# Kernel optimization log

Hardware: AMD Instinct MI355X
Metric: run time of the kernel (lower is better)

The kernel has to match this reference:

```python
import jax, jax.numpy as jnp
import numpy as np

N = 50000      # nodes
E = 1_600_000  # edges
F_IN = 128     # in_dim
H = 4          # heads
C = 32         # hidden_dim per head  (H*C == 128)
G = 64         # graphs in batch
HID2 = 64      # 2*hidden_dim
OUT = 10       # output_dim


def seg_softmax(logits, seg, num):
    # softmax over entries sharing the same segment id (leading axis)
    m = jax.ops.segment_max(logits, seg, num_segments=num)
    e = jnp.exp(logits - m[seg])
    s = jax.ops.segment_sum(e, seg, num_segments=num)
    return e / s[seg]


def gat_conv(x, src, dst, W, a_src, a_dst, b):
    # PyG GATConv (concat=True, negative_slope=0.2, self-loops added)
    h = (x @ W).reshape(N, H, C)                     # [N,H,C]
    loop = jnp.arange(N, dtype=src.dtype)
    s = jnp.concatenate([src, loop])                 # [E+N]
    d = jnp.concatenate([dst, loop])
    al_s = jnp.sum(h * a_src[None], axis=-1)         # [N,H]
    al_d = jnp.sum(h * a_dst[None], axis=-1)
    logits = jax.nn.leaky_relu(al_s[s] + al_d[d], 0.2)   # [E+N,H]
    alpha = seg_softmax(logits, d, N)                # softmax over incoming edges per dst
    msg = alpha[:, :, None] * h[s]                   # [E+N,H,C]
    out = jax.ops.segment_sum(msg, d, num_segments=N)    # [N,H,C]
    return out.reshape(N, H * C) + b


def setup_inputs() -> dict:
    key = jax.random.key(0)
    ks = jax.random.split(key, 16)
    x = jax.random.normal(ks[0], (N, F_IN), dtype=jnp.float32)
    src = jax.random.randint(ks[1], (E,), 0, N, dtype=jnp.int64)
    dst = jax.random.randint(ks[2], (E,), 0, N, dtype=jnp.int64)
    dst = jnp.where(src == dst, (dst + 1) % N, dst)  # GATConv removes self-loops then re-adds them
    edge_index = jnp.stack([src, dst])
    batch = jnp.sort(jax.random.randint(ks[3], (N,), 0, G, dtype=jnp.int64))
    g = lambda k, shp, fan: jax.random.normal(k, shp, dtype=jnp.float32) / np.sqrt(fan)
    return {
        "x": x, "edge_index": edge_index, "batch": batch,
        "W1": g(ks[4], (F_IN, H * C), F_IN), "a_src1": g(ks[5], (H, C), C), "a_dst1": g(ks[6], (H, C), C), "b1": jnp.zeros((H * C,), jnp.float32),
        "W2": g(ks[7], (H * C, H * C), H * C), "a_src2": g(ks[8], (H, C), C), "a_dst2": g(ks[9], (H, C), C), "b2": jnp.zeros((H * C,), jnp.float32),
        "gate_w": g(ks[10], (H * C, 1), H * C), "gate_b": jnp.zeros((1,), jnp.float32),
        "lin_w": g(ks[11], (H * C, HID2), H * C), "lin_b": jnp.zeros((HID2,), jnp.float32),
        "cls_w": g(ks[12], (HID2, OUT), HID2), "cls_b": jnp.zeros((OUT,), jnp.float32),
    }


def reference(x, edge_index, batch, W1, a_src1, a_dst1, b1, W2, a_src2, a_dst2, b2,
              gate_w, gate_b, lin_w, lin_b, cls_w, cls_b):
    src, dst = edge_index[0], edge_index[1]
    layers = [(W1, a_src1, a_dst1, b1), (W2, a_src2, a_dst2, b2)]
    hg = None
    h = x
    for (W, a_s, a_d, b) in layers:
        h = gat_conv(h, src, dst, W, a_s, a_d, b)
        h = jax.nn.relu(h)
        # per-graph softmax over nodes (dim=0 within each graph), per feature column
        h = seg_softmax(h, batch, G)
        # GlobalAttention pooling: gated segment-softmax sum
        gate = h @ gate_w + gate_b                    # [N,1]
        gate = seg_softmax(gate, batch, G)
        pooled = jax.ops.segment_sum(gate * h, batch, num_segments=G)  # [G, H*C]
        hg = pooled if hg is None else hg + pooled
    out = jax.nn.relu(hg @ lin_w + lin_b)             # dropout is identity in eval mode
    out = out @ cls_w + cls_b                         # [G, OUT]
    return out
```

## Files before the change

### kernel.cpp

```cpp
#include <hip/hip_runtime.h>
#include <hip/hip_fp16.h>
#include <math.h>

constexpr int N    = 50000;
constexpr int E    = 1600000;
constexpr int FD   = 128;
constexpr int H    = 4;
constexpr int G    = 64;
constexpr int NCH  = 16;
constexpr int OUT  = 10;

constexpr int NBIN   = (N + 255) / 256;
constexpr int EPB    = 4096;
constexpr int NBLK_E = (E + EPB - 1) / EPB;

#define DEV __device__ __forceinline__

DEV void fma4(float4& a, float s, const float4& w) {
    a.x = fmaf(s, w.x, a.x); a.y = fmaf(s, w.y, a.y);
    a.z = fmaf(s, w.z, a.z); a.w = fmaf(s, w.w, a.w);
}

DEV float lrelu_exp(float z) {
    return __expf(z > 0.f ? z : 0.2f * z);
}

union HF4 {
    float2  f;
    __half2 h[2];
};

DEV void fmah(float4& a, float w, const HF4& u) {
    float2 lo = __half22float2(u.h[0]);
    float2 hi = __half22float2(u.h[1]);
    a.x = fmaf(w, lo.x, a.x); a.y = fmaf(w, lo.y, a.y);
    a.z = fmaf(w, hi.x, a.z); a.w = fmaf(w, hi.y, a.w);
}


__global__ void k_zero(int* __restrict__ hist, float* __restrict__ hg) {
    int i = blockIdx.x * 256 + threadIdx.x;
    if (i < NBIN) hist[i] = 0;
    if (i < G * FD) hg[i] = 0.f;
}

__global__ void k_graph_starts(const int* __restrict__ batch, int* __restrict__ gs) {
    int i = blockIdx.x * 256 + threadIdx.x;
    if (i >= N) return;
    int b  = batch[i];
    int pb = (i == 0) ? -1 : batch[i - 1];
    for (int g = pb + 1; g <= b; ++g) gs[g] = i;
    if (i == N - 1) for (int g = b + 1; g <= G; ++g) gs[g] = N;
}

__global__ __launch_bounds__(256)
void k_hist(const int* __restrict__ dst, int* __restrict__ hist) {
    __shared__ int lh[NBIN];
    int t = threadIdx.x;
    for (int i = t; i < NBIN; i += 256) lh[i] = 0;
    __syncthreads();
    int base = blockIdx.x * EPB;
#pragma unroll
    for (int j = 0; j < EPB / 256; ++j) {
        int e = base + j * 256 + t;
        if (e < E) atomicAdd(&lh[dst[e] >> 8], 1);
    }
    __syncthreads();
    for (int i = t; i < NBIN; i += 256) if (lh[i]) atomicAdd(&hist[i], lh[i]);
}

__global__ __launch_bounds__(256)
void k_binscan(const int* __restrict__ hist, int* __restrict__ binbase,
               int* __restrict__ cursor, int* __restrict__ off) {
    __shared__ int sh[256];
    int t = threadIdx.x;
    int v = (t < NBIN) ? hist[t] : 0;
    sh[t] = v;
    __syncthreads();
    for (int d = 1; d < 256; d <<= 1) {
        int add = (t >= d) ? sh[t - d] : 0;
        __syncthreads();
        sh[t] += add;
        __syncthreads();
    }
    if (t < NBIN) {
        binbase[t] = sh[t] - v;
        cursor[t]  = sh[t] - v;
    }
    if (t == NBIN - 1) binbase[NBIN] = sh[t];
    if (t == 0) off[N] = E;
}

__global__ __launch_bounds__(256)
void k_partition(const int* __restrict__ src, const int* __restrict__ dst,
                 int* __restrict__ cursor, unsigned int* __restrict__ part) {
    __shared__ int lh[NBIN];
    __shared__ int gb[NBIN];
    int t = threadIdx.x;
    for (int i = t; i < NBIN; i += 256) lh[i] = 0;
    __syncthreads();
    int base = blockIdx.x * EPB;
    unsigned int pk[EPB / 256];
    int          pr[EPB / 256];
#pragma unroll
    for (int j = 0; j < EPB / 256; ++j) {
        int e = base + j * 256 + t;
        if (e < E) {
            int d = dst[e];
            int b = d >> 8;
            int r = atomicAdd(&lh[b], 1);
            pk[j] = (unsigned)src[e] | ((unsigned)(d & 255) << 16);
            pr[j] = (b << 16) | r;
        } else pr[j] = -1;
    }
    __syncthreads();
    for (int i = t; i < NBIN; i += 256) gb[i] = atomicAdd(&cursor[i], lh[i]);
    __syncthreads();
#pragma unroll
    for (int j = 0; j < EPB / 256; ++j) {
        if (pr[j] >= 0) {
            int b = pr[j] >> 16, r = pr[j] & 0xFFFF;
            part[gb[b] + r] = pk[j];
        }
    }
}

__global__ __launch_bounds__(256)
void k_fine(const unsigned int* __restrict__ part, const int* __restrict__ binbase,
            int* __restrict__ off, int* __restrict__ col) {
    __shared__ int lh[256], lo[256], lc[256];
    int b = blockIdx.x, t = threadIdx.x;
    int s = binbase[b], e = binbase[b + 1];
    lh[t] = 0; lc[t] = 0;
    __syncthreads();
    for (int i = s + t; i < e; i += 256) atomicAdd(&lh[part[i] >> 16], 1);
    __syncthreads();
    int v = lh[t];
    lo[t] = v;
    __syncthreads();
    for (int d = 1; d < 256; d <<= 1) {
        int add = (t >= d) ? lo[t - d] : 0;
        __syncthreads();
        lo[t] += add;
        __syncthreads();
    }
    int ex = lo[t] - v;
    __syncthreads();
    lo[t] = ex;
    __syncthreads();
    int node = b * 256 + t;
    if (node < N) off[node] = s + ex;
    for (int i = s + t; i < e; i += 256) {
        unsigned p = part[i];
        int dl = p >> 16;
        int r = atomicAdd(&lc[dl], 1);
        col[s + lo[dl] + r] = (int)(p & 0xFFFFu);
    }
}

__global__ __launch_bounds__(256, 2)
void k_gemm_al(const float* __restrict__ X, const float* __restrict__ W,
               const float* __restrict__ a_s, const float* __restrict__ a_d,
               __half* __restrict__ hw, float* __restrict__ als, float* __restrict__ ald)
{
    __shared__ float xs[128][128];
    int r0 = blockIdx.x * 128;
    int t  = threadIdx.x;

    for (int i = 0; i < 16; ++i) {
        int f   = i * 256 + t;
        int row = f >> 5;
        int colf = (f & 31) * 4;
        float4 v = make_float4(0.f, 0.f, 0.f, 0.f);
        if (r0 + row < N) v = *(const float4*)(X + (size_t)(r0 + row) * FD + colf);
        *(float4*)(&xs[row][colf]) = v;
    }
    __syncthreads();

    int ct = t & 31;
    int rt = t >> 5;
    int c4 = ct * 4;
    int rb = rt * 16;

    float4 acc[16];
#pragma unroll
    for (int r = 0; r < 16; ++r) acc[r] = make_float4(0.f, 0.f, 0.f, 0.f);

    for (int k = 0; k < FD; k += 4) {
        float4 wv0 = *(const float4*)(W + (size_t)(k + 0) * FD + c4);
        float4 wv1 = *(const float4*)(W + (size_t)(k + 1) * FD + c4);
        float4 wv2 = *(const float4*)(W + (size_t)(k + 2) * FD + c4);
        float4 wv3 = *(const float4*)(W + (size_t)(k + 3) * FD + c4);
#pragma unroll
        for (int r = 0; r < 16; ++r) {
            float4 xv = *(const float4*)(&xs[rb + r][k]);
            fma4(acc[r], xv.x, wv0);
            fma4(acc[r], xv.y, wv1);
            fma4(acc[r], xv.z, wv2);
            fma4(acc[r], xv.w, wv3);
        }
    }

    int h  = c4 >> 5;
    int j0 = c4 & 31;
    float as0 = a_s[h * 32 + j0 + 0], as1 = a_s[h * 32 + j0 + 1];
    float as2 = a_s[h * 32 + j0 + 2], as3 = a_s[h * 32 + j0 + 3];
    float ad0 = a_d[h * 32 + j0 + 0], ad1 = a_d[h * 32 + j0 + 1];
    float ad2 = a_d[h * 32 + j0 + 2], ad3 = a_d[h * 32 + j0 + 3];

#pragma unroll
    for (int r = 0; r < 16; ++r) {
        int row = r0 + rb + r;
        bool valid = row < N;
        if (valid) {
            HF4 u;
            u.h[0] = __floats2half2_rn(acc[r].x, acc[r].y);
            u.h[1] = __floats2half2_rn(acc[r].z, acc[r].w);
            *(float2*)(hw + (size_t)row * FD + c4) = u.f;
        }
        float ps = acc[r].x * as0 + acc[r].y * as1 + acc[r].z * as2 + acc[r].w * as3;
        float pd = acc[r].x * ad0 + acc[r].y * ad1 + acc[r].z * ad2 + acc[r].w * ad3;
#pragma unroll
        for (int m = 1; m < 8; m <<= 1) {
            ps += __shfl_xor(ps, m, 64);
            pd += __shfl_xor(pd, m, 64);
        }
        if ((ct & 7) == 0 && valid) {
            als[row * H + h] = ps;
            ald[row * H + h] = pd;
        }
    }
}

__global__ __launch_bounds__(256)
void k_agg(const __half* __restrict__ hw, const float* __restrict__ als,
           const float* __restrict__ ald, const int* __restrict__ off,
           const int* __restrict__ col, const float* __restrict__ bias,
           float* __restrict__ h1)
{
    int n = blockIdx.x * 4 + (threadIdx.x >> 6);
    if (n >= N) return;
    int l = threadIdx.x & 63;
    int q = l >> 5;
    int p = l & 31;
    int h = p >> 3;
    float adn = ald[n * H + h];

    float4 acc = make_float4(0.f, 0.f, 0.f, 0.f);
    float sumw;
    {
        float w = q ? 0.f : lrelu_exp(als[n * H + h] + adn);
        HF4 u; u.f = *(const float2*)(hw + (size_t)n * FD + 4 * p);
        fmah(acc, w, u);
        sumw = w;
    }

    int ib = off[n];
    int deg = off[n + 1] - ib;
    int j = 0;
    for (; j + 8 <= deg; j += 8) {
        int s0 = col[ib + j + 0 + q];
        int s1 = col[ib + j + 2 + q];
        int s2 = col[ib + j + 4 + q];
        int s3 = col[ib + j + 6 + q];
        float z0 = als[s0 * H + h];
        float z1 = als[s1 * H + h];
        float z2 = als[s2 * H + h];
        float z3 = als[s3 * H + h];
        HF4 u0; u0.f = *(const float2*)(hw + (size_t)s0 * FD + 4 * p);
        HF4 u1; u1.f = *(const float2*)(hw + (size_t)s1 * FD + 4 * p);
        HF4 u2; u2.f = *(const float2*)(hw + (size_t)s2 * FD + 4 * p);
        HF4 u3; u3.f = *(const float2*)(hw + (size_t)s3 * FD + 4 * p);
        float w0 = lrelu_exp(z0 + adn);
        float w1 = lrelu_exp(z1 + adn);
        float w2 = lrelu_exp(z2 + adn);
        float w3 = lrelu_exp(z3 + adn);
        fmah(acc, w0, u0);
        fmah(acc, w1, u1);
        fmah(acc, w2, u2);
        fmah(acc, w3, u3);
        sumw += w0 + w1 + w2 + w3;
    }
    for (; j + 2 <= deg; j += 2) {
        int s = col[ib + j + q];
        float w = lrelu_exp(als[s * H + h] + adn);
        HF4 u; u.f = *(const float2*)(hw + (size_t)s * FD + 4 * p);
        fmah(acc, w, u);
        sumw += w;
    }
    if (j < deg) {
        int s = q ? n : col[ib + j];
        float w = q ? 0.f : lrelu_exp(als[s * H + h] + adn);
        HF4 u; u.f = *(const float2*)(hw + (size_t)s * FD + 4 * p);
        fmah(acc, w, u);
        sumw += w;
    }

    acc.x += __shfl_xor(acc.x, 32, 64);
    acc.y += __shfl_xor(acc.y, 32, 64);
    acc.z += __shfl_xor(acc.z, 32, 64);
    acc.w += __shfl_xor(acc.w, 32, 64);
    sumw  += __shfl_xor(sumw,  32, 64);

    if (q == 0) {
        float inv = 1.f / sumw;
        float4 b4 = *(const float4*)(bias + 4 * p);
        float4 o;
        o.x = fmaf(acc.x, inv, b4.x);
        o.y = fmaf(acc.y, inv, b4.y);
        o.z = fmaf(acc.z, inv, b4.z);
        o.w = fmaf(acc.w, inv, b4.w);
        o.x = o.x > 0.f ? o.x : 0.f;
        o.y = o.y > 0.f ? o.y : 0.f;
        o.z = o.z > 0.f ? o.z : 0.f;
        o.w = o.w > 0.f ? o.w : 0.f;
        *(float4*)(h1 + (size_t)n * FD + 4 * p) = o;
    }
}

__global__ void k_colstats_part(const float* __restrict__ h1, const int* __restrict__ gs,
                                float* __restrict__ Mp, float* __restrict__ Sp)
{
    int g = blockIdx.x, ch = blockIdx.y, c = threadIdx.x;
    int s = gs[g], e = gs[g + 1];
    int per = (e - s + NCH - 1) / NCH;
    int ns = s + ch * per;
    int ne = min(ns + per, e);
    float m = -3e38f;
    for (int n = ns; n < ne; ++n) m = fmaxf(m, h1[(size_t)n * FD + c]);
    float sum = 0.f;
    for (int n = ns; n < ne; ++n) sum += __expf(h1[(size_t)n * FD + c] - m);
    int o = (g * NCH + ch) * FD + c;
    Mp[o] = m; Sp[o] = sum;
}

__global__ void k_colstats_comb(const float* __restrict__ Mp, const float* __restrict__ Sp,
                                float* __restrict__ Mm, float* __restrict__ Sinv)
{
    int g = blockIdx.x, c = threadIdx.x;
    float m = -3e38f;
#pragma unroll
    for (int ch = 0; ch < NCH; ++ch) m = fmaxf(m, Mp[(g * NCH + ch) * FD + c]);
    float s = 0.f;
#pragma unroll
    for (int ch = 0; ch < NCH; ++ch) {
        float sp = Sp[(g * NCH + ch) * FD + c];
        if (sp > 0.f) s += sp * __expf(Mp[(g * NCH + ch) * FD + c] - m);
    }
    Mm[g * FD + c] = m;
    Sinv[g * FD + c] = 1.f / s;
}

__global__ __launch_bounds__(256)
void k_softmax_gate(const float* __restrict__ h1, const int* __restrict__ batch,
                    const float* __restrict__ Mm, const float* __restrict__ Sinv,
                    const float* __restrict__ gw, const float* __restrict__ gb,
                    float* __restrict__ hsm, float* __restrict__ gl)
{
    int n = blockIdx.x * 4 + (threadIdx.x >> 6);
    if (n >= N) return;
    int l = threadIdx.x & 63;
    int g = batch[n];
    float2 hv = *(const float2*)(h1 + (size_t)n * FD + 2 * l);
    float2 mv = *(const float2*)(Mm + g * FD + 2 * l);
    float2 sv = *(const float2*)(Sinv + g * FD + 2 * l);
    float vx = __expf(hv.x - mv.x) * sv.x;
    float vy = __expf(hv.y - mv.y) * sv.y;
    float2 o = make_float2(vx, vy);
    *(float2*)(hsm + (size_t)n * FD + 2 * l) = o;
    float p = vx * gw[2 * l] + vy * gw[2 * l + 1];
#pragma unroll
    for (int m = 1; m < 64; m <<= 1) p += __shfl_xor(p, m, 64);
    if (l == 0) gl[n] = p + gb[0];
}

__global__ __launch_bounds__(256)
void k_gatestats(const float* __restrict__ gl, const int* __restrict__ gs,
                 float* __restrict__ Mg, float* __restrict__ iSg)
{
    __shared__ float red[8];
    int g = blockIdx.x;
    int s = gs[g], e = gs[g + 1];
    int t = threadIdx.x;
    float m = -3e38f;
    for (int i = s + t; i < e; i += 256) m = fmaxf(m, gl[i]);
#pragma unroll
    for (int mk = 1; mk < 64; mk <<= 1) m = fmaxf(m, __shfl_xor(m, mk, 64));
    if ((t & 63) == 0) red[t >> 6] = m;
    __syncthreads();
    if (t == 0) {
        float mm = red[0];
        for (int w2 = 1; w2 < 4; ++w2) mm = fmaxf(mm, red[w2]);
        red[0] = mm;
    }
    __syncthreads();
    m = red[0];
    float sum = 0.f;
    for (int i = s + t; i < e; i += 256) sum += __expf(gl[i] - m);
#pragma unroll
    for (int mk = 1; mk < 64; mk <<= 1) sum += __shfl_xor(sum, mk, 64);
    if ((t & 63) == 0) red[4 + (t >> 6)] = sum;
    __syncthreads();
    if (t == 0) {
        float ss = red[4] + red[5] + red[6] + red[7];
        Mg[g] = m;
        iSg[g] = 1.f / ss;
    }
}

__global__ void k_pool(const float* __restrict__ hsm, const float* __restrict__ gl,
                       const int* __restrict__ gs, const float* __restrict__ Mg,
                       const float* __restrict__ iSg, float* __restrict__ hg)
{
    int g = blockIdx.x, ch = blockIdx.y, c = threadIdx.x;
    int s = gs[g], e = gs[g + 1];
    int per = (e - s + NCH - 1) / NCH;
    int ns = s + ch * per;
    int ne = min(ns + per, e);
    float mg = Mg[g], is = iSg[g];
    float acc = 0.f;
    for (int n = ns; n < ne; ++n)
        acc = fmaf(__expf(gl[n] - mg) * is, hsm[(size_t)n * FD + c], acc);
    atomicAdd(&hg[g * FD + c], acc);
}

__global__ __launch_bounds__(64)
void k_head(const float* __restrict__ hg, const float* __restrict__ lin_w,
            const float* __restrict__ lin_b, const float* __restrict__ cls_w,
            const float* __restrict__ cls_b, float* __restrict__ out)
{
    __shared__ float hrow[128];
    __shared__ float tbuf[64];
    int g = blockIdx.x, j = threadIdx.x;
    hrow[j]      = hg[g * FD + j];
    hrow[j + 64] = hg[g * FD + j + 64];
    __syncthreads();
    float a = lin_b[j];
    for (int c = 0; c < 128; ++c) a = fmaf(hrow[c], lin_w[c * 64 + j], a);
    tbuf[j] = a > 0.f ? a : 0.f;
    __syncthreads();
    if (j < OUT) {
        float o = cls_b[j];
        for (int k = 0; k < 64; ++k) o = fmaf(tbuf[k], cls_w[k * OUT + j], o);
        out[g * OUT + j] = o;
    }
}

extern "C" void kernel_launch(void* const* d_in, const int* in_sizes, int n_in,
                              void* d_out, int out_size, void* d_ws, size_t ws_size,
                              hipStream_t stream)
{
    const float* x      = (const float*)d_in[0];
    const int*   ei     = (const int*)d_in[1];
    const int*   src    = ei;
    const int*   dst    = ei + E;
    const int*   batch  = (const int*)d_in[2];
    const float* W1     = (const float*)d_in[3];
    const float* as1    = (const float*)d_in[4];
    const float* ad1    = (const float*)d_in[5];
    const float* b1     = (const float*)d_in[6];
    const float* W2     = (const float*)d_in[7];
    const float* as2    = (const float*)d_in[8];
    const float* ad2    = (const float*)d_in[9];
    const float* b2     = (const float*)d_in[10];
    const float* gate_w = (const float*)d_in[11];
    const float* gate_b = (const float*)d_in[12];
    const float* lin_w  = (const float*)d_in[13];
    const float* lin_b  = (const float*)d_in[14];
    const float* cls_w  = (const float*)d_in[15];
    const float* cls_b  = (const float*)d_in[16];
    float* outp = (float*)d_out;

    char* ws = (char*)d_ws;
    size_t o = 0;
    auto alloc = [&](size_t bytes) -> char* {
        char* p = ws + o;
        o = (o + bytes + 255) & ~(size_t)255;
        return p;
    };

    int*    gs      = (int*)alloc((G + 1) * sizeof(int));
    int*    hist    = (int*)alloc(256 * sizeof(int));
    int*    binbase = (int*)alloc(256 * sizeof(int));
    int*    cursor  = (int*)alloc(256 * sizeof(int));
    int*    off     = (int*)alloc((N + 1) * sizeof(int));
    int*    col     = (int*)alloc((size_t)E * sizeof(int));
    float*  als     = (float*)alloc((size_t)N * H * sizeof(float));
    float*  ald     = (float*)alloc((size_t)N * H * sizeof(float));
    __half* hw      = (__half*)alloc((size_t)N * FD * sizeof(__half));
    float*  h1      = (float*)alloc((size_t)N * FD * sizeof(float));
    float*  hsm     = (float*)alloc((size_t)N * FD * sizeof(float));
    float*  Mp      = (float*)alloc((size_t)G * NCH * FD * sizeof(float));
    float*  Sp      = (float*)alloc((size_t)G * NCH * FD * sizeof(float));
    float*  Mm      = (float*)alloc((size_t)G * FD * sizeof(float));
    float*  Sinv    = (float*)alloc((size_t)G * FD * sizeof(float));
    float*  gl      = (float*)alloc((size_t)N * sizeof(float));
    float*  Mg      = (float*)alloc(G * sizeof(float));
    float*  iSg     = (float*)alloc(G * sizeof(float));
    float*  hg      = (float*)alloc((size_t)G * FD * sizeof(float));

    unsigned int* part = (unsigned int*)hw;

    int nbN = (N + 255) / 256;

    k_zero<<<32, 256, 0, stream>>>(hist, hg);
    k_graph_starts<<<nbN, 256, 0, stream>>>(batch, gs);
    k_hist<<<NBLK_E, 256, 0, stream>>>(dst, hist);
    k_binscan<<<1, 256, 0, stream>>>(hist, binbase, cursor, off);
    k_partition<<<NBLK_E, 256, 0, stream>>>(src, dst, cursor, part);
    k_fine<<<NBIN, 256, 0, stream>>>(part, binbase, off, col);

    auto run_layer = [&](const float* hin, const float* W, const float* a_s,
                         const float* a_d, const float* bias) {
        k_gemm_al<<<(N + 127) / 128, 256, 0, stream>>>(hin, W, a_s, a_d, hw, als, ald);
        k_agg<<<(N + 3) / 4, 256, 0, stream>>>(hw, als, ald, off, col, bias, h1);
        k_colstats_part<<<dim3(G, NCH), 128, 0, stream>>>(h1, gs, Mp, Sp);
        k_colstats_comb<<<G, 128, 0, stream>>>(Mp, Sp, Mm, Sinv);
        k_softmax_gate<<<(N + 3) / 4, 256, 0, stream>>>(h1, batch, Mm, Sinv, gate_w, gate_b, hsm, gl);
        k_gatestats<<<G, 256, 0, stream>>>(gl, gs, Mg, iSg);
        k_pool<<<dim3(G, NCH), 128, 0, stream>>>(hsm, gl, gs, Mg, iSg, hg);
    };

    run_layer(x, W1, as1, ad1, b1);
    run_layer(hsm, W2, as2, ad2, b2);

    k_head<<<G, 64, 0, stream>>>(hg, lin_w, lin_b, cls_w, cls_b, outp);
}
```

Measured before the change: 459.8 us.

## Drop max-subtraction in softmaxes, store activations in fp16, merge stats kernels

Removes the max pass from both the per-graph column softmax and the gate softmax, summing exp values directly with atomics. That collapses colstats_part/comb and gatestats into a single colsum kernel plus atomic accumulation inside the gate kernel. The h1 and hsm activations are now stored as fp16, so the gemm reads half input for layer 2. Less memory traffic and fewer launches, at the cost of overflow risk without max subtraction (bounded only because values are post-ReLU or softmax outputs in [0,1]), plus fp16 precision loss and non-deterministic atomics.

```diff
diff --git a/kernel.cpp b/kernel.cpp
--- a/kernel.cpp
+++ b/kernel.cpp
@@ -37,11 +37,22 @@
     a.z = fmaf(w, hi.x, a.z); a.w = fmaf(w, hi.y, a.w);
 }
 
-
-__global__ void k_zero(int* __restrict__ hist, float* __restrict__ hg) {
+DEV float4 load4f(const float* p) { return *(const float4*)p; }
+DEV float4 load4f(const __half* p) {
+    HF4 u; u.f = *(const float2*)p;
+    float2 lo = __half22float2(u.h[0]);
+    float2 hi = __half22float2(u.h[1]);
+    return make_float4(lo.x, lo.y, hi.x, hi.y);
+}
+
+
+__global__ void k_zero(int* __restrict__ hist, float* __restrict__ hg,
+                       float* __restrict__ S1, float* __restrict__ S2,
+                       float* __restrict__ Eg1, float* __restrict__ Eg2) {
     int i = blockIdx.x * 256 + threadIdx.x;
     if (i < NBIN) hist[i] = 0;
-    if (i < G * FD) hg[i] = 0.f;
+    if (i < G * FD) { hg[i] = 0.f; S1[i] = 0.f; S2[i] = 0.f; }
+    if (i < G) { Eg1[i] = 0.f; Eg2[i] = 0.f; }
 }
 
 __global__ void k_graph_starts(const int* __restrict__ batch, int* __restrict__ gs) {
@@ -158,8 +169,9 @@
     }
 }
 
+template <typename TIn>
 __global__ __launch_bounds__(256, 2)
-void k_gemm_al(const float* __restrict__ X, const float* __restrict__ W,
+void k_gemm_al(const TIn* __restrict__ X, const float* __restrict__ W,
                const float* __restrict__ a_s, const float* __restrict__ a_d,
                __half* __restrict__ hw, float* __restrict__ als, float* __restrict__ ald)
 {
@@ -172,7 +184,7 @@
         int row = f >> 5;
         int colf = (f & 31) * 4;
         float4 v = make_float4(0.f, 0.f, 0.f, 0.f);
-        if (r0 + row < N) v = *(const float4*)(X + (size_t)(r0 + row) * FD + colf);
+        if (r0 + row < N) v = load4f(X + (size_t)(r0 + row) * FD + colf);
         *(float4*)(&xs[row][colf]) = v;
     }
     __syncthreads();
@@ -236,7 +248,7 @@
 void k_agg(const __half* __restrict__ hw, const float* __restrict__ als,
            const float* __restrict__ ald, const int* __restrict__ off,
            const int* __restrict__ col, const float* __restrict__ bias,
-           float* __restrict__ h1)
+           __half* __restrict__ h1)
 {
     int n = blockIdx.x * 4 + (threadIdx.x >> 6);
     if (n >= N) return;
@@ -314,114 +326,73 @@
         o.y = o.y > 0.f ? o.y : 0.f;
         o.z = o.z > 0.f ? o.z : 0.f;
         o.w = o.w > 0.f ? o.w : 0.f;
-        *(float4*)(h1 + (size_t)n * FD + 4 * p) = o;
-    }
-}
-
-__global__ void k_colstats_part(const float* __restrict__ h1, const int* __restrict__ gs,
-                                float* __restrict__ Mp, float* __restrict__ Sp)
-{
-    int g = blockIdx.x, ch = blockIdx.y, c = threadIdx.x;
+        HF4 u;
+        u.h[0] = __floats2half2_rn(o.x, o.y);
+        u.h[1] = __floats2half2_rn(o.z, o.w);
+        *(float2*)(h1 + (size_t)n * FD + 4 * p) = u.f;
+    }
+}
+
+__global__ __launch_bounds__(256)
+void k_colsum(const __half* __restrict__ h1, const int* __restrict__ gs,
+              float* __restrict__ S)
+{
+    int g = blockIdx.x, ch = blockIdx.y;
+    int t = threadIdx.x;
+    int c = t & 127, hf = t >> 7;
     int s = gs[g], e = gs[g + 1];
     int per = (e - s + NCH - 1) / NCH;
     int ns = s + ch * per;
     int ne = min(ns + per, e);
-    float m = -3e38f;
-    for (int n = ns; n < ne; ++n) m = fmaxf(m, h1[(size_t)n * FD + c]);
     float sum = 0.f;
-    for (int n = ns; n < ne; ++n) sum += __expf(h1[(size_t)n * FD + c] - m);
-    int o = (g * NCH + ch) * FD + c;
-    Mp[o] = m; Sp[o] = sum;
-}
-
-__global__ void k_colstats_comb(const float* __restrict__ Mp, const float* __restrict__ Sp,
-                                float* __restrict__ Mm, float* __restrict__ Sinv)
-{
-    int g = blockIdx.x, c = threadIdx.x;
-    float m = -3e38f;
-#pragma unroll
-    for (int ch = 0; ch < NCH; ++ch) m = fmaxf(m, Mp[(g * NCH + ch) * FD + c]);
-    float s = 0.f;
-#pragma unroll
-    for (int ch = 0; ch < NCH; ++ch) {
-        float sp = Sp[(g * NCH + ch) * FD + c];
-        if (sp > 0.f) s += sp * __expf(Mp[(g * NCH + ch) * FD + c] - m);
-    }
-    Mm[g * FD + c] = m;
-    Sinv[g * FD + c] = 1.f / s;
-}
-
-__global__ __launch_bounds__(256)
-void k_softmax_gate(const float* __restrict__ h1, const int* __restrict__ batch,
-                    const float* __restrict__ Mm, const float* __restrict__ Sinv,
-                    const float* __restrict__ gw, const float* __restrict__ gb,
-                    float* __restrict__ hsm, float* __restrict__ gl)
+    for (int n = ns + hf; n < ne; n += 2)
+        sum += __expf(__half2float(h1[(size_t)n * FD + c]));
+    if (sum > 0.f) atomicAdd(&S[g * FD + c], sum);
+}
+
+__global__ __launch_bounds__(256)
+void k_softmax_gate(const __half* __restrict__ h1, const int* __restrict__ batch,
+                    const float* __restrict__ S, const float* __restrict__ gw,
+                    const float* __restrict__ gb, __half* __restrict__ hsm,
+                    float* __restrict__ egl, float* __restrict__ Eg)
 {
     int n = blockIdx.x * 4 + (threadIdx.x >> 6);
     if (n >= N) return;
     int l = threadIdx.x & 63;
     int g = batch[n];
-    float2 hv = *(const float2*)(h1 + (size_t)n * FD + 2 * l);
-    float2 mv = *(const float2*)(Mm + g * FD + 2 * l);
-    float2 sv = *(const float2*)(Sinv + g * FD + 2 * l);
-    float vx = __expf(hv.x - mv.x) * sv.x;
-    float vy = __expf(hv.y - mv.y) * sv.y;
-    float2 o = make_float2(vx, vy);
-    *(float2*)(hsm + (size_t)n * FD + 2 * l) = o;
+    float2 hv = __half22float2(*(const __half2*)(h1 + (size_t)n * FD + 2 * l));
+    float2 sv = *(const float2*)(S + g * FD + 2 * l);
+    float vx = __expf(hv.x) / sv.x;
+    float vy = __expf(hv.y) / sv.y;
+    *(__half2*)(hsm + (size_t)n * FD + 2 * l) = __floats2half2_rn(vx, vy);
     float p = vx * gw[2 * l] + vy * gw[2 * l + 1];
 #pragma unroll
     for (int m = 1; m < 64; m <<= 1) p += __shfl_xor(p, m, 64);
-    if (l == 0) gl[n] = p + gb[0];
-}
-
-__global__ __launch_bounds__(256)
-void k_gatestats(const float* __restrict__ gl, const int* __restrict__ gs,
-                 float* __restrict__ Mg, float* __restrict__ iSg)
-{
-    __shared__ float red[8];
-    int g = blockIdx.x;
-    int s = gs[g], e = gs[g + 1];
+    if (l == 0) {
+        float eg = __expf(p + gb[0]);
+        egl[n] = eg;
+        atomicAdd(&Eg[g], eg);
+    }
+}
+
+__global__ __launch_bounds__(256)
+void k_pool(const __half* __restrict__ hsm, const float* __restrict__ egl,
+            const int* __restrict__ gs, const float* __restrict__ Eg,
+            float* __restrict__ hg)
+{
+    int g = blockIdx.x, ch = blockIdx.y;
     int t = threadIdx.x;
-    float m = -3e38f;
-    for (int i = s + t; i < e; i += 256) m = fmaxf(m, gl[i]);
-#pragma unroll
-    for (int mk = 1; mk < 64; mk <<= 1) m = fmaxf(m, __shfl_xor(m, mk, 64));
-    if ((t & 63) == 0) red[t >> 6] = m;
-    __syncthreads();
-    if (t == 0) {
-        float mm = red[0];
-        for (int w2 = 1; w2 < 4; ++w2) mm = fmaxf(mm, red[w2]);
-        red[0] = mm;
-    }
-    __syncthreads();
-    m = red[0];
-    float sum = 0.f;
-    for (int i = s + t; i < e; i += 256) sum += __expf(gl[i] - m);
-#pragma unroll
-    for (int mk = 1; mk < 64; mk <<= 1) sum += __shfl_xor(sum, mk, 64);
-    if ((t & 63) == 0) red[4 + (t >> 6)] = sum;
-    __syncthreads();
-    if (t == 0) {
-        float ss = red[4] + red[5] + red[6] + red[7];
-        Mg[g] = m;
-        iSg[g] = 1.f / ss;
-    }
-}
-
-__global__ void k_pool(const float* __restrict__ hsm, const float* __restrict__ gl,
-                       const int* __restrict__ gs, const float* __restrict__ Mg,
-                       const float* __restrict__ iSg, float* __restrict__ hg)
-{
-    int g = blockIdx.x, ch = blockIdx.y, c = threadIdx.x;
+    int c = t & 127, hf = t >> 7;
     int s = gs[g], e = gs[g + 1];
     int per = (e - s + NCH - 1) / NCH;
     int ns = s + ch * per;
     int ne = min(ns + per, e);
-    float mg = Mg[g], is = iSg[g];
+    if (ns >= ne) return;
+    float inv = 1.f / Eg[g];
     float acc = 0.f;
-    for (int n = ns; n < ne; ++n)
-        acc = fmaf(__expf(gl[n] - mg) * is, hsm[(size_t)n * FD + c], acc);
-    atomicAdd(&hg[g * FD + c], acc);
+    for (int n = ns + hf; n < ne; n += 2)
+        acc = fmaf(egl[n], __half2float(hsm[(size_t)n * FD + c]), acc);
+    atomicAdd(&hg[g * FD + c], acc * inv);
 }
 
 __global__ __launch_bounds__(64)
@@ -488,41 +459,37 @@
     float*  als     = (float*)alloc((size_t)N * H * sizeof(float));
     float*  ald     = (float*)alloc((size_t)N * H * sizeof(float));
     __half* hw      = (__half*)alloc((size_t)N * FD * sizeof(__half));
-    float*  h1      = (float*)alloc((size_t)N * FD * sizeof(float));
-    float*  hsm     = (float*)alloc((size_t)N * FD * sizeof(float));
-    float*  Mp      = (float*)alloc((size_t)G * NCH * FD * sizeof(float));
-    float*  Sp      = (float*)alloc((size_t)G * NCH * FD * sizeof(float));
-    float*  Mm      = (float*)alloc((size_t)G * FD * sizeof(float));
-    float*  Sinv    = (float*)alloc((size_t)G * FD * sizeof(float));
-    float*  gl      = (float*)alloc((size_t)N * sizeof(float));
-    float*  Mg      = (float*)alloc(G * sizeof(float));
-    float*  iSg     = (float*)alloc(G * sizeof(float));
+    __half* h1      = (__half*)alloc((size_t)N * FD * sizeof(__half));
+    __half* hsm     = (__half*)alloc((size_t)N * FD * sizeof(__half));
+    float*  S1      = (float*)alloc((size_t)G * FD * sizeof(float));
+    float*  S2      = (float*)alloc((size_t)G * FD * sizeof(float));
+    float*  Eg1     = (float*)alloc(G * sizeof(float));
+    float*  Eg2     = (float*)alloc(G * sizeof(float));
+    float*  egl     = (float*)alloc((size_t)N * sizeof(float));
     float*  hg      = (float*)alloc((size_t)G * FD * sizeof(float));
 
     unsigned int* part = (unsigned int*)hw;
 
     int nbN = (N + 255) / 256;
 
-    k_zero<<<32, 256, 0, stream>>>(hist, hg);
+    k_zero<<<32, 256, 0, stream>>>(hist, hg, S1, S2, Eg1, Eg2);
     k_graph_starts<<<nbN, 256, 0, stream>>>(batch, gs);
     k_hist<<<NBLK_E, 256, 0, stream>>>(dst, hist);
     k_binscan<<<1, 256, 0, stream>>>(hist, binbase, cursor, off);
     k_partition<<<NBLK_E, 256, 0, stream>>>(src, dst, cursor, part);
     k_fine<<<NBIN, 256, 0, stream>>>(part, binbase, off, col);
 
-    auto run_layer = [&](const float* hin, const float* W, const float* a_s,
-                         const float* a_d, const float* bias) {
+    auto run_layer = [&](auto hin, const float* W, const float* a_s,
+                         const float* a_d, const float* bias, float* S, float* Eg) {
         k_gemm_al<<<(N + 127) / 128, 256, 0, stream>>>(hin, W, a_s, a_d, hw, als, ald);
         k_agg<<<(N + 3) / 4, 256, 0, stream>>>(hw, als, ald, off, col, bias, h1);
-        k_colstats_part<<<dim3(G, NCH), 128, 0, stream>>>(h1, gs, Mp, Sp);
-        k_colstats_comb<<<G, 128, 0, stream>>>(Mp, Sp, Mm, Sinv);
-        k_softmax_gate<<<(N + 3) / 4, 256, 0, stream>>>(h1, batch, Mm, Sinv, gate_w, gate_b, hsm, gl);
-        k_gatestats<<<G, 256, 0, stream>>>(gl, gs, Mg, iSg);
-        k_pool<<<dim3(G, NCH), 128, 0, stream>>>(hsm, gl, gs, Mg, iSg, hg);
+        k_colsum<<<dim3(G, NCH), 256, 0, stream>>>(h1, gs, S);
+        k_softmax_gate<<<(N + 3) / 4, 256, 0, stream>>>(h1, batch, S, gate_w, gate_b, hsm, egl, Eg);
+        k_pool<<<dim3(G, NCH), 256, 0, stream>>>(hsm, egl, gs, Eg, hg);
     };
 
-    run_layer(x, W1, as1, ad1, b1);
-    run_layer(hsm, W2, as2, ad2, b2);
+    run_layer(x, W1, as1, ad1, b1, S1, Eg1);
+    run_layer((const __half*)hsm, W2, as2, ad2, b2, S2, Eg2);
 
     k_head<<<G, 64, 0, stream>>>(hg, lin_w, lin_b, cls_w, cls_b, outp);
 }
```

Measured after the change: 1.167 ms. 2.54x slower.
